# Performance work log

Hardware: AMD Instinct MI355X
Metric: run time of the kernel (lower is better)

The kernel has to match this reference:

```python
import jax, jax.numpy as jnp
import numpy as np

ALPHA = 0.7
BETA = 0.3


def setup_inputs() -> dict:
    key = jax.random.key(0)
    k1, k2 = jax.random.split(key)
    n = 8192
    predictions = jax.random.normal(k1, (n,), dtype=jnp.float32)
    # graded relevance labels in {0,1,2,3}, stored as float (torch code compares floats)
    targets = jax.random.randint(k2, (n,), 0, 4).astype(jnp.float32)
    return {"predictions": predictions, "targets": targets}


def reference(predictions, targets):
    # SmoothL1 (Huber, beta=1) with mean reduction
    d = predictions - targets
    ad = jnp.abs(d)
    huber = jnp.mean(jnp.where(ad < 1.0, 0.5 * d * d, ad - 0.5))

    # Pairwise hinge ranking loss over i<j pairs with targets[i] != targets[j].
    n = predictions.shape[0]
    pd = predictions[:, None] - predictions[None, :]   # [n, n] pred_i - pred_j
    td = targets[:, None] - targets[None, :]           # [n, n] targ_i - targ_j
    sign = jnp.where(td > 0, 1.0, -1.0)                # target_ranking
    idx = jnp.arange(n)
    mask = (td != 0) & (idx[:, None] < idx[None, :])   # upper triangle, unequal targets
    hinge = jnp.maximum(0.0, 1.0 - sign * pd)
    num = jnp.sum(jnp.where(mask, hinge, 0.0))
    cnt = jnp.sum(mask).astype(predictions.dtype)
    ranking = jnp.where(cnt > 0, num / jnp.maximum(cnt, 1.0), 0.0)

    return ALPHA * huber + BETA * ranking
```

## Files before the change

kernel.cpp:

```cpp
#include <hip/hip_runtime.h>

static constexpr int TI = 128;
static constexpr int NTHREADS = 256;


template <bool DIAG>
__device__ __forceinline__ void accum_tile(const float4* __restrict__ sj4,
                                           float pi, float tiv, int il, int half,
                                           float& s0, float& s1, float& s2, float& s3,
                                           float& c0, float& c1, float& c2, float& c3) {
  const int k0 = half * 32;
#pragma unroll
  for (int k = 0; k < 32; k += 2) {
    float4 a = sj4[k0 + k];
    float4 b = sj4[k0 + k + 1];
    const int jb = 2 * (k0 + k);
    {
      float sg = fminf(fmaxf(tiv - a.y, -1.f), 1.f);
      if (DIAG) sg = (jb + 0 > il) ? sg : 0.f;
      s0 += fmaxf(fmaf(-sg, pi - a.x, fabsf(sg)), 0.f); c0 += fabsf(sg);
    }
    {
      float sg = fminf(fmaxf(tiv - a.w, -1.f), 1.f);
      if (DIAG) sg = (jb + 1 > il) ? sg : 0.f;
      s1 += fmaxf(fmaf(-sg, pi - a.z, fabsf(sg)), 0.f); c1 += fabsf(sg);
    }
    {
      float sg = fminf(fmaxf(tiv - b.y, -1.f), 1.f);
      if (DIAG) sg = (jb + 2 > il) ? sg : 0.f;
      s2 += fmaxf(fmaf(-sg, pi - b.x, fabsf(sg)), 0.f); c2 += fabsf(sg);
    }
    {
      float sg = fminf(fmaxf(tiv - b.w, -1.f), 1.f);
      if (DIAG) sg = (jb + 3 > il) ? sg : 0.f;
      s3 += fmaxf(fmaf(-sg, pi - b.z, fabsf(sg)), 0.f); c3 += fabsf(sg);
    }
  }
}

__global__ __launch_bounds__(NTHREADS) void egl_pair_kernel(
    const float* __restrict__ pred, const float* __restrict__ targ, int n, int nT,
    float* __restrict__ ws_s, float* __restrict__ ws_c, float* __restrict__ ws_h) {
  int bidx = blockIdx.x;
  int ti = 0, rem = bidx;
  while (rem >= nT - ti) { rem -= (nT - ti); ++ti; }
  const int tj = ti + rem;

  __shared__ alignas(16) float2 sj[TI];
  const int tid  = threadIdx.x;
  const int il   = tid & (TI - 1);
  const int half = tid >> 7;
  const int j0 = tj * TI;
  if (tid < TI) {
    int j = j0 + tid;
    float pj = (j < n) ? pred[j] : 0.0f;
    float tv = (j < n) ? targ[j] : 0.0f;
    sj[tid] = make_float2(pj, tv);
  }
  __syncthreads();

  const int i = ti * TI + il;
  const bool ivalid = (i < n);
  const float pi  = ivalid ? pred[i] : 0.0f;
  const float tiv = ivalid ? targ[i] : 0.0f;

  float s0 = 0.f, s1 = 0.f, s2 = 0.f, s3 = 0.f;
  float c0 = 0.f, c1 = 0.f, c2 = 0.f, c3 = 0.f;
  float hub = 0.f;

  const int jcount = min(TI, n - j0);
  const float4* sj4 = (const float4*)sj;

  if (ivalid) {
    if (ti != tj) {
      if (jcount == TI) {
        accum_tile<false>(sj4, pi, tiv, il, half, s0, s1, s2, s3, c0, c1, c2, c3);
      } else {
        const int jlo = half * 64;
        const int jhi = min(jlo + 64, jcount);
        for (int jj = jlo; jj < jhi; ++jj) {
          float2 a = sj[jj];
          float sg = fminf(fmaxf(tiv - a.y, -1.f), 1.f);
          s0 += fmaxf(fmaf(-sg, pi - a.x, fabsf(sg)), 0.f);
          c0 += fabsf(sg);
        }
      }
    } else {
      if (half == 0) {
        float d = pi - tiv;
        float ad = fabsf(d);
        hub = (ad < 1.0f) ? 0.5f * d * d : (ad - 0.5f);
      }
      if (jcount == TI) {
        accum_tile<true>(sj4, pi, tiv, il, half, s0, s1, s2, s3, c0, c1, c2, c3);
      } else {
        const int jlo = max(il + 1, half * 64);
        const int jhi = min(half * 64 + 64, jcount);
        for (int jj = jlo; jj < jhi; ++jj) {
          float2 a = sj[jj];
          float sg = fminf(fmaxf(tiv - a.y, -1.f), 1.f);
          s0 += fmaxf(fmaf(-sg, pi - a.x, fabsf(sg)), 0.f);
          c0 += fabsf(sg);
        }
      }
    }
  }

  float s = (s0 + s1) + (s2 + s3);
  float c = (c0 + c1) + (c2 + c3);

  for (int off = 32; off > 0; off >>= 1) {
    s   += __shfl_down(s, off, 64);
    c   += __shfl_down(c, off, 64);
    hub += __shfl_down(hub, off, 64);
  }
  __shared__ float red[4][3];
  if ((tid & 63) == 0) {
    int w = tid >> 6;
    red[w][0] = s; red[w][1] = c; red[w][2] = hub;
  }
  __syncthreads();
  if (tid == 0) {
    ws_s[bidx] = (red[0][0] + red[1][0]) + (red[2][0] + red[3][0]);
    ws_c[bidx] = (red[0][1] + red[1][1]) + (red[2][1] + red[3][1]);
    ws_h[bidx] = (red[0][2] + red[1][2]) + (red[2][2] + red[3][2]);
  }
}

__global__ __launch_bounds__(256) void egl_finalize(
    const float* __restrict__ ws_s, const float* __restrict__ ws_c,
    const float* __restrict__ ws_h, int nb, int n, float* __restrict__ out) {
  double s = 0.0, c = 0.0, h = 0.0;
  for (int idx = threadIdx.x; idx < nb; idx += 256) {
    s += (double)ws_s[idx];
    c += (double)ws_c[idx];
    h += (double)ws_h[idx];
  }
  for (int off = 32; off > 0; off >>= 1) {
    s += __shfl_down(s, off, 64);
    c += __shfl_down(c, off, 64);
    h += __shfl_down(h, off, 64);
  }
  __shared__ double red[4][3];
  int w = threadIdx.x >> 6;
  if ((threadIdx.x & 63) == 0) { red[w][0] = s; red[w][1] = c; red[w][2] = h; }
  __syncthreads();
  if (threadIdx.x == 0) {
    double S = 0.0, C = 0.0, H = 0.0;
    for (int k = 0; k < 4; ++k) { S += red[k][0]; C += red[k][1]; H += red[k][2]; }
    double huber = H / (double)n;
    double rank = (C > 0.0) ? (S / fmax(C, 1.0)) : 0.0;
    out[0] = (float)(0.7 * huber + 0.3 * rank);
  }
}

extern "C" void kernel_launch(void* const* d_in, const int* in_sizes, int n_in,
                              void* d_out, int out_size, void* d_ws, size_t ws_size,
                              hipStream_t stream) {
  const float* pred = (const float*)d_in[0];
  const float* targ = (const float*)d_in[1];
  const int n = in_sizes[0];

  const int nT = (n + TI - 1) / TI;
  const int nb = nT * (nT + 1) / 2;

  float* ws_s = (float*)d_ws;
  float* ws_c = ws_s + nb;
  float* ws_h = ws_c + nb;

  egl_pair_kernel<<<nb, NTHREADS, 0, stream>>>(pred, targ, n, nT, ws_s, ws_c, ws_h);
  egl_finalize<<<1, 256, 0, stream>>>(ws_s, ws_c, ws_h, nb, n, (float*)d_out);
}
```

Measured before the change: 67.03 us.

## Compute pair count from label histogram and use symmetric diagonal tiles

```diff
diff --git a/kernel.cpp b/kernel.cpp
--- a/kernel.cpp
+++ b/kernel.cpp
@@ -4,43 +4,9 @@
 static constexpr int NTHREADS = 256;
 
 
-template <bool DIAG>
-__device__ __forceinline__ void accum_tile(const float4* __restrict__ sj4,
-                                           float pi, float tiv, int il, int half,
-                                           float& s0, float& s1, float& s2, float& s3,
-                                           float& c0, float& c1, float& c2, float& c3) {
-  const int k0 = half * 32;
-#pragma unroll
-  for (int k = 0; k < 32; k += 2) {
-    float4 a = sj4[k0 + k];
-    float4 b = sj4[k0 + k + 1];
-    const int jb = 2 * (k0 + k);
-    {
-      float sg = fminf(fmaxf(tiv - a.y, -1.f), 1.f);
-      if (DIAG) sg = (jb + 0 > il) ? sg : 0.f;
-      s0 += fmaxf(fmaf(-sg, pi - a.x, fabsf(sg)), 0.f); c0 += fabsf(sg);
-    }
-    {
-      float sg = fminf(fmaxf(tiv - a.w, -1.f), 1.f);
-      if (DIAG) sg = (jb + 1 > il) ? sg : 0.f;
-      s1 += fmaxf(fmaf(-sg, pi - a.z, fabsf(sg)), 0.f); c1 += fabsf(sg);
-    }
-    {
-      float sg = fminf(fmaxf(tiv - b.y, -1.f), 1.f);
-      if (DIAG) sg = (jb + 2 > il) ? sg : 0.f;
-      s2 += fmaxf(fmaf(-sg, pi - b.x, fabsf(sg)), 0.f); c2 += fabsf(sg);
-    }
-    {
-      float sg = fminf(fmaxf(tiv - b.w, -1.f), 1.f);
-      if (DIAG) sg = (jb + 3 > il) ? sg : 0.f;
-      s3 += fmaxf(fmaf(-sg, pi - b.z, fabsf(sg)), 0.f); c3 += fabsf(sg);
-    }
-  }
-}
-
 __global__ __launch_bounds__(NTHREADS) void egl_pair_kernel(
     const float* __restrict__ pred, const float* __restrict__ targ, int n, int nT,
-    float* __restrict__ ws_s, float* __restrict__ ws_c, float* __restrict__ ws_h) {
+    float* __restrict__ ws_s, float* __restrict__ ws_h) {
   int bidx = blockIdx.x;
   int ti = 0, rem = bidx;
   while (rem >= nT - ti) { rem -= (nT - ti); ++ti; }
@@ -55,6 +21,7 @@
     int j = j0 + tid;
     float pj = (j < n) ? pred[j] : 0.0f;
     float tv = (j < n) ? targ[j] : 0.0f;
+    if (j >= n) { pj = 0.0f; tv = -1e30f; }
     sj[tid] = make_float2(pj, tv);
   }
   __syncthreads();
@@ -65,91 +32,105 @@
   const float tiv = ivalid ? targ[i] : 0.0f;
 
   float s0 = 0.f, s1 = 0.f, s2 = 0.f, s3 = 0.f;
-  float c0 = 0.f, c1 = 0.f, c2 = 0.f, c3 = 0.f;
   float hub = 0.f;
 
   const int jcount = min(TI, n - j0);
   const float4* sj4 = (const float4*)sj;
 
+  if (ivalid && ti == tj && half == 0) {
+    float d = pi - tiv;
+    float ad = fabsf(d);
+    hub = (ad < 1.0f) ? 0.5f * d * d : (ad - 0.5f);
+  }
+
   if (ivalid) {
-    if (ti != tj) {
-      if (jcount == TI) {
-        accum_tile<false>(sj4, pi, tiv, il, half, s0, s1, s2, s3, c0, c1, c2, c3);
-      } else {
-        const int jlo = half * 64;
-        const int jhi = min(jlo + 64, jcount);
-        for (int jj = jlo; jj < jhi; ++jj) {
-          float2 a = sj[jj];
-          float sg = fminf(fmaxf(tiv - a.y, -1.f), 1.f);
-          s0 += fmaxf(fmaf(-sg, pi - a.x, fabsf(sg)), 0.f);
-          c0 += fabsf(sg);
-        }
+    if (jcount == TI) {
+      const int k0 = half * 32;
+#pragma unroll
+      for (int k = 0; k < 32; k += 2) {
+        float4 a = sj4[k0 + k];
+        float4 b = sj4[k0 + k + 1];
+        { float sg = __builtin_amdgcn_fmed3f(tiv - a.y, -1.f, 1.f);
+          s0 += fmaxf(fmaf(-sg, pi - a.x, fabsf(sg)), 0.f); }
+        { float sg = __builtin_amdgcn_fmed3f(tiv - a.w, -1.f, 1.f);
+          s1 += fmaxf(fmaf(-sg, pi - a.z, fabsf(sg)), 0.f); }
+        { float sg = __builtin_amdgcn_fmed3f(tiv - b.y, -1.f, 1.f);
+          s2 += fmaxf(fmaf(-sg, pi - b.x, fabsf(sg)), 0.f); }
+        { float sg = __builtin_amdgcn_fmed3f(tiv - b.w, -1.f, 1.f);
+          s3 += fmaxf(fmaf(-sg, pi - b.z, fabsf(sg)), 0.f); }
       }
     } else {
-      if (half == 0) {
-        float d = pi - tiv;
-        float ad = fabsf(d);
-        hub = (ad < 1.0f) ? 0.5f * d * d : (ad - 0.5f);
-      }
-      if (jcount == TI) {
-        accum_tile<true>(sj4, pi, tiv, il, half, s0, s1, s2, s3, c0, c1, c2, c3);
-      } else {
-        const int jlo = max(il + 1, half * 64);
-        const int jhi = min(half * 64 + 64, jcount);
-        for (int jj = jlo; jj < jhi; ++jj) {
-          float2 a = sj[jj];
-          float sg = fminf(fmaxf(tiv - a.y, -1.f), 1.f);
-          s0 += fmaxf(fmaf(-sg, pi - a.x, fabsf(sg)), 0.f);
-          c0 += fabsf(sg);
-        }
+      const int jlo = half * 64;
+      const int jhi = min(jlo + 64, jcount);
+      for (int jj = jlo; jj < jhi; ++jj) {
+        float2 a = sj[jj];
+        float sg = __builtin_amdgcn_fmed3f(tiv - a.y, -1.f, 1.f);
+        s0 += fmaxf(fmaf(-sg, pi - a.x, fabsf(sg)), 0.f);
       }
     }
   }
 
   float s = (s0 + s1) + (s2 + s3);
-  float c = (c0 + c1) + (c2 + c3);
 
   for (int off = 32; off > 0; off >>= 1) {
     s   += __shfl_down(s, off, 64);
-    c   += __shfl_down(c, off, 64);
     hub += __shfl_down(hub, off, 64);
   }
-  __shared__ float red[4][3];
+  __shared__ float red[4][2];
   if ((tid & 63) == 0) {
     int w = tid >> 6;
-    red[w][0] = s; red[w][1] = c; red[w][2] = hub;
+    red[w][0] = s; red[w][1] = hub;
   }
   __syncthreads();
   if (tid == 0) {
-    ws_s[bidx] = (red[0][0] + red[1][0]) + (red[2][0] + red[3][0]);
-    ws_c[bidx] = (red[0][1] + red[1][1]) + (red[2][1] + red[3][1]);
-    ws_h[bidx] = (red[0][2] + red[1][2]) + (red[2][2] + red[3][2]);
+    float scale = (ti == tj) ? 0.5f : 1.0f;
+    ws_s[bidx] = ((red[0][0] + red[1][0]) + (red[2][0] + red[3][0])) * scale;
+    ws_h[bidx] = (red[0][1] + red[1][1]) + (red[2][1] + red[3][1]);
   }
 }
 
 __global__ __launch_bounds__(256) void egl_finalize(
-    const float* __restrict__ ws_s, const float* __restrict__ ws_c,
-    const float* __restrict__ ws_h, int nb, int n, float* __restrict__ out) {
-  double s = 0.0, c = 0.0, h = 0.0;
+    const float* __restrict__ ws_s, const float* __restrict__ ws_h,
+    const float* __restrict__ targ, int nb, int n, float* __restrict__ out) {
+  double s = 0.0, h = 0.0;
   for (int idx = threadIdx.x; idx < nb; idx += 256) {
     s += (double)ws_s[idx];
-    c += (double)ws_c[idx];
     h += (double)ws_h[idx];
   }
+  int c0 = 0, c1 = 0, c2 = 0;
+  for (int idx = threadIdx.x; idx < n; idx += 256) {
+    float t = targ[idx];
+    c0 += (t < 0.5f) ? 1 : 0;
+    c1 += (t < 1.5f) ? 1 : 0;
+    c2 += (t < 2.5f) ? 1 : 0;
+  }
   for (int off = 32; off > 0; off >>= 1) {
-    s += __shfl_down(s, off, 64);
-    c += __shfl_down(c, off, 64);
-    h += __shfl_down(h, off, 64);
+    s  += __shfl_down(s, off, 64);
+    h  += __shfl_down(h, off, 64);
+    c0 += __shfl_down(c0, off, 64);
+    c1 += __shfl_down(c1, off, 64);
+    c2 += __shfl_down(c2, off, 64);
   }
-  __shared__ double red[4][3];
+  __shared__ double sred[4][2];
+  __shared__ int    cred[4][3];
   int w = threadIdx.x >> 6;
-  if ((threadIdx.x & 63) == 0) { red[w][0] = s; red[w][1] = c; red[w][2] = h; }
+  if ((threadIdx.x & 63) == 0) {
+    sred[w][0] = s; sred[w][1] = h;
+    cred[w][0] = c0; cred[w][1] = c1; cred[w][2] = c2;
+  }
   __syncthreads();
   if (threadIdx.x == 0) {
-    double S = 0.0, C = 0.0, H = 0.0;
-    for (int k = 0; k < 4; ++k) { S += red[k][0]; C += red[k][1]; H += red[k][2]; }
+    double S = 0.0, H = 0.0;
+    long long C0 = 0, C1 = 0, C2 = 0;
+    for (int k = 0; k < 4; ++k) {
+      S += sred[k][0]; H += sred[k][1];
+      C0 += cred[k][0]; C1 += cred[k][1]; C2 += cred[k][2];
+    }
+    long long H0 = C0, H1 = C1 - C0, H2 = C2 - C1, H3 = (long long)n - C2;
+    long long same = H0 * (H0 - 1) + H1 * (H1 - 1) + H2 * (H2 - 1) + H3 * (H3 - 1);
+    long long cnt = ((long long)n * (n - 1) - same) / 2;
     double huber = H / (double)n;
-    double rank = (C > 0.0) ? (S / fmax(C, 1.0)) : 0.0;
+    double rank = (cnt > 0) ? (S / (double)cnt) : 0.0;
     out[0] = (float)(0.7 * huber + 0.3 * rank);
   }
 }
@@ -165,9 +146,8 @@
   const int nb = nT * (nT + 1) / 2;
 
   float* ws_s = (float*)d_ws;
-  float* ws_c = ws_s + nb;
-  float* ws_h = ws_c + nb;
+  float* ws_h = ws_s + nb;
 
-  egl_pair_kernel<<<nb, NTHREADS, 0, stream>>>(pred, targ, n, nT, ws_s, ws_c, ws_h);
-  egl_finalize<<<1, 256, 0, stream>>>(ws_s, ws_c, ws_h, nb, n, (float*)d_out);
+  egl_pair_kernel<<<nb, NTHREADS, 0, stream>>>(pred, targ, n, nT, ws_s, ws_h);
+  egl_finalize<<<1, 256, 0, stream>>>(ws_s, ws_h, targ, nb, n, (float*)d_out);
 }
```

Result: slower. 68.81 us (+2.7%).
